# Performance work log

Measured on AMD Instinct MI355X. Metric: run time of the kernel, lower is better.

The kernel has to match this reference:

```python
import jax, jax.numpy as jnp
import numpy as np

B, T, E = 1024, 200, 128
H = 64

def setup_inputs() -> dict:
    key = jax.random.key(0)
    k1, k2, k3, k4 = jax.random.split(key, 4)
    return {
        "query": jax.random.normal(k1, (B, 1, E), dtype=jnp.float32),
        "keys": jax.random.normal(k2, (B, T, E), dtype=jnp.float32),
        "W0": jax.random.normal(k3, (4 * E, H), dtype=jnp.float32) * 0.05,
        "b0": jnp.zeros((H,), dtype=jnp.float32),
        "W1": jax.random.normal(k4, (H, 1), dtype=jnp.float32) * 0.05,
        "b1": jnp.zeros((1,), dtype=jnp.float32),
    }

def reference(query, keys, W0, b0, W1, b1):
    # query: [B,1,E] broadcast to [B,T,E] (repeat_elements along axis 1)
    q = jnp.broadcast_to(query, keys.shape)
    # dnn_input: [B,T,4E] = concat([q, k, q-k, q*k])
    x = jnp.concatenate([q, keys, q - keys, q * keys], axis=-1)
    # one hidden layer with relu, then linear scorer -> [B,T,1]
    h = jax.nn.relu(jnp.einsum('btd,dh->bth', x, W0) + b0)
    att_score = jnp.einsum('bth,ho->bto', h, W1) + b1
    return att_score
```

## Files before the change

### kernel.cpp

```cpp
#include <hip/hip_runtime.h>
#include <hip/hip_bf16.h>


#define TB 200
#define EB 128
#define HB 64

typedef __attribute__((ext_vector_type(8))) short bf16x8;
typedef __attribute__((ext_vector_type(4))) float f32x4;

__global__ __launch_bounds__(256, 4)
void lau_kernel(const float* __restrict__ query,
                const float* __restrict__ keys,
                const float* __restrict__ W0,
                const float* __restrict__ b0,
                const float* __restrict__ W1,
                const float* __restrict__ b1,
                float* __restrict__ out)
{
    const int b    = blockIdx.x;
    const int tid  = threadIdx.x;
    const int lane = tid & 63;
    const int wave = tid >> 6;
    const int ln15 = lane & 15;
    const int quad = lane >> 4;

    __shared__ float bias_s[HB];
    __shared__ float w1_s[HB];
    __shared__ float red2[HB][17];
    __shared__ __align__(16) __hip_bfloat16 wbt[HB][EB + 8];

    const float* kb = keys + (size_t)b * TB * EB;

    {
        const int hq = (tid & 15) * 4;
        const int ck = tid >> 4;
        const float4 q0 = *(const float4*)&query[(size_t)b * EB + ck * 8];
        const float4 q1 = *(const float4*)&query[(size_t)b * EB + ck * 8 + 4];
        const float qe_arr[8] = {q0.x, q0.y, q0.z, q0.w, q1.x, q1.y, q1.z, q1.w};
        float bp0 = 0.f, bp1 = 0.f, bp2 = 0.f, bp3 = 0.f;
        #pragma unroll
        for (int i = 0; i < 8; ++i) {
            const int e = ck * 8 + i;
            const float qe = qe_arr[i];
            const float4 wa = *(const float4*)&W0[(size_t)e            * HB + hq];
            const float4 wb = *(const float4*)&W0[(size_t)(EB + e)     * HB + hq];
            const float4 wc = *(const float4*)&W0[(size_t)(2 * EB + e) * HB + hq];
            const float4 wd = *(const float4*)&W0[(size_t)(3 * EB + e) * HB + hq];
            wbt[hq + 0][e] = __float2bfloat16(wb.x - wc.x + qe * wd.x);
            wbt[hq + 1][e] = __float2bfloat16(wb.y - wc.y + qe * wd.y);
            wbt[hq + 2][e] = __float2bfloat16(wb.z - wc.z + qe * wd.z);
            wbt[hq + 3][e] = __float2bfloat16(wb.w - wc.w + qe * wd.w);
            bp0 += qe * (wa.x + wc.x);
            bp1 += qe * (wa.y + wc.y);
            bp2 += qe * (wa.z + wc.z);
            bp3 += qe * (wa.w + wc.w);
        }
        red2[hq + 0][ck] = bp0;
        red2[hq + 1][ck] = bp1;
        red2[hq + 2][ck] = bp2;
        red2[hq + 3][ck] = bp3;
    }

    float4 af[8];
    {
        const int mrow = wave * 16 + ln15;
        const float* arow = kb + (size_t)mrow * EB + quad * 8;
        #pragma unroll
        for (int ks = 0; ks < 4; ++ks) {
            af[2*ks]   = *(const float4*)(arow + ks * 32);
            af[2*ks+1] = *(const float4*)(arow + ks * 32 + 4);
        }
    }
    __syncthreads();

    if (tid < HB) {
        float s = b0[tid];
        #pragma unroll
        for (int c = 0; c < 16; ++c) s += red2[tid][c];
        bias_s[tid] = s;
        w1_s[tid]   = W1[tid];
    }
    __syncthreads();

    float w1q[4], biasq[4];
    #pragma unroll
    for (int nt = 0; nt < 4; ++nt) {
        w1q[nt]   = w1_s[nt * 16 + ln15];
        biasq[nt] = bias_s[nt * 16 + ln15];
    }

    const __hip_bfloat16* wb_base = &wbt[ln15][quad * 8];
    const float b1v = b1[0];

    for (int mt = wave; mt < 13; mt += 4) {
        bf16x8 ab[4];
        #pragma unroll
        for (int ks = 0; ks < 4; ++ks) {
            union { bf16x8 v; __hip_bfloat162 h2[4]; } u;
            u.h2[0] = __float22bfloat162_rn(make_float2(af[2*ks].x,   af[2*ks].y));
            u.h2[1] = __float22bfloat162_rn(make_float2(af[2*ks].z,   af[2*ks].w));
            u.h2[2] = __float22bfloat162_rn(make_float2(af[2*ks+1].x, af[2*ks+1].y));
            u.h2[3] = __float22bfloat162_rn(make_float2(af[2*ks+1].z, af[2*ks+1].w));
            ab[ks] = u.v;
        }

        if (mt + 4 < 13) {
            const int mrow = (mt + 4) * 16 + ln15;
            const int mc   = mrow < TB ? mrow : TB - 1;
            const float* arow = kb + (size_t)mc * EB + quad * 8;
            #pragma unroll
            for (int ks = 0; ks < 4; ++ks) {
                af[2*ks]   = *(const float4*)(arow + ks * 32);
                af[2*ks+1] = *(const float4*)(arow + ks * 32 + 4);
            }
        }

        f32x4 acc[4] = {{0,0,0,0},{0,0,0,0},{0,0,0,0},{0,0,0,0}};
        #pragma unroll
        for (int ks = 0; ks < 4; ++ks) {
            #pragma unroll
            for (int nt = 0; nt < 4; ++nt) {
                const bf16x8 bf = *(const bf16x8*)(wb_base + nt * 16 * (EB + 8) + ks * 32);
                acc[nt] = __builtin_amdgcn_mfma_f32_16x16x32_bf16(ab[ks], bf, acc[nt], 0, 0, 0);
            }
        }

        float part[4];
        #pragma unroll
        for (int r = 0; r < 4; ++r) {
            float s = 0.f;
            #pragma unroll
            for (int nt = 0; nt < 4; ++nt) {
                float hv = acc[nt][r] + biasq[nt];
                hv = hv > 0.f ? hv : 0.f;
                s += hv * w1q[nt];
            }
            part[r] = s;
        }
        #pragma unroll
        for (int m = 1; m < 16; m <<= 1) {
            #pragma unroll
            for (int r = 0; r < 4; ++r)
                part[r] += __shfl_xor(part[r], m, 64);
        }
        if (ln15 == 0) {
            #pragma unroll
            for (int r = 0; r < 4; ++r) {
                const int mg = mt * 16 + quad * 4 + r;
                if (mg < TB) out[(size_t)b * TB + mg] = part[r] + b1v;
            }
        }
    }
}

extern "C" void kernel_launch(void* const* d_in, const int* in_sizes, int n_in,
                              void* d_out, int out_size, void* d_ws, size_t ws_size,
                              hipStream_t stream) {
    const float* query = (const float*)d_in[0];
    const float* keys  = (const float*)d_in[1];
    const float* W0    = (const float*)d_in[2];
    const float* b0    = (const float*)d_in[3];
    const float* W1    = (const float*)d_in[4];
    const float* b1    = (const float*)d_in[5];
    float* out = (float*)d_out;

    lau_kernel<<<1024, 256, 0, stream>>>(query, keys, W0, b0, W1, b1, out);
}
```

Measured before the change: 181.0 us.

## Split weight folding into separate kernel and halve per-batch score blocks

Moves the per-batch query-folded W0 computation into its own kernel that writes bf16 weights and bias to a workspace. The scoring kernel then runs two blocks per batch, each handling about half of the 13 row tiles, and reloads the folded weights from the workspace. The aim is more parallelism, with the fold work kept off the critical path of the key-streaming GEMM. In exchange it adds a second launch, roughly 18MB of extra workspace traffic, and drops the software prefetch of the next key tile.

```diff
diff --git a/kernel.cpp b/kernel.cpp
--- a/kernel.cpp
+++ b/kernel.cpp
@@ -5,32 +5,23 @@
 #define TB 200
 #define EB 128
 #define HB 64
+#define WS_STRIDE 17664
 
 typedef __attribute__((ext_vector_type(8))) short bf16x8;
 typedef __attribute__((ext_vector_type(4))) float f32x4;
 
 __global__ __launch_bounds__(256, 4)
-void lau_kernel(const float* __restrict__ query,
-                const float* __restrict__ keys,
-                const float* __restrict__ W0,
-                const float* __restrict__ b0,
-                const float* __restrict__ W1,
-                const float* __restrict__ b1,
-                float* __restrict__ out)
+void fold_kernel(const float* __restrict__ query,
+                 const float* __restrict__ W0,
+                 const float* __restrict__ b0,
+                 unsigned char* __restrict__ ws)
 {
-    const int b    = blockIdx.x;
-    const int tid  = threadIdx.x;
-    const int lane = tid & 63;
-    const int wave = tid >> 6;
-    const int ln15 = lane & 15;
-    const int quad = lane >> 4;
+    const int b   = blockIdx.x;
+    const int tid = threadIdx.x;
 
+    __shared__ float red2[HB][17];
     __shared__ float bias_s[HB];
-    __shared__ float w1_s[HB];
-    __shared__ float red2[HB][17];
     __shared__ __align__(16) __hip_bfloat16 wbt[HB][EB + 8];
-
-    const float* kb = keys + (size_t)b * TB * EB;
 
     {
         const int hq = (tid & 15) * 4;
@@ -61,24 +52,50 @@
         red2[hq + 2][ck] = bp2;
         red2[hq + 3][ck] = bp3;
     }
-
-    float4 af[8];
-    {
-        const int mrow = wave * 16 + ln15;
-        const float* arow = kb + (size_t)mrow * EB + quad * 8;
-        #pragma unroll
-        for (int ks = 0; ks < 4; ++ks) {
-            af[2*ks]   = *(const float4*)(arow + ks * 32);
-            af[2*ks+1] = *(const float4*)(arow + ks * 32 + 4);
-        }
-    }
     __syncthreads();
-
     if (tid < HB) {
         float s = b0[tid];
         #pragma unroll
         for (int c = 0; c < 16; ++c) s += red2[tid][c];
         bias_s[tid] = s;
+    }
+    __syncthreads();
+
+    uint4* dst = (uint4*)(ws + (size_t)b * WS_STRIDE);
+    const uint4* srcW = (const uint4*)&wbt[0][0];
+    #pragma unroll
+    for (int k = 0; k < 4; ++k) dst[tid + k * 256] = srcW[tid + k * 256];
+    if (tid < 64) dst[1024 + tid] = srcW[1024 + tid];
+    if (tid < 16) dst[1088 + tid] = ((const uint4*)bias_s)[tid];
+}
+
+__global__ __launch_bounds__(256, 8)
+void score_kernel(const float* __restrict__ keys,
+                  const float* __restrict__ W1,
+                  const float* __restrict__ b1,
+                  const unsigned char* __restrict__ ws,
+                  float* __restrict__ out)
+{
+    const int bid  = blockIdx.x;
+    const int b    = bid >> 1;
+    const int half = bid & 1;
+    const int tid  = threadIdx.x;
+    const int lane = tid & 63;
+    const int wave = tid >> 6;
+    const int ln15 = lane & 15;
+    const int quad = lane >> 4;
+
+    __shared__ float bias_s[HB];
+    __shared__ float w1_s[HB];
+    __shared__ __align__(16) __hip_bfloat16 wbt[HB][EB + 8];
+
+    const uint4* src = (const uint4*)(ws + (size_t)b * WS_STRIDE);
+    uint4* dstW = (uint4*)&wbt[0][0];
+    #pragma unroll
+    for (int k = 0; k < 4; ++k) dstW[tid + k * 256] = src[tid + k * 256];
+    if (tid < 64) dstW[1024 + tid] = src[1024 + tid];
+    if (tid < 64) {
+        bias_s[tid] = ((const float*)(ws + (size_t)b * WS_STRIDE + 17408))[tid];
         w1_s[tid]   = W1[tid];
     }
     __syncthreads();
@@ -91,9 +108,21 @@
     }
 
     const __hip_bfloat16* wb_base = &wbt[ln15][quad * 8];
-    const float b1v = b1[0];
+    const float* kb  = keys + (size_t)b * TB * EB;
+    const float  b1v = b1[0];
 
-    for (int mt = wave; mt < 13; mt += 4) {
+    const int mtEnd = half ? 13 : 7;
+    for (int mt = half * 7 + wave; mt < mtEnd; mt += 4) {
+        const int mrow = mt * 16 + ln15;
+        const int mc   = mrow < TB ? mrow : TB - 1;
+        const float* arow = kb + (size_t)mc * EB + quad * 8;
+
+        float4 af[8];
+        #pragma unroll
+        for (int ks = 0; ks < 4; ++ks) {
+            af[2*ks]   = *(const float4*)(arow + ks * 32);
+            af[2*ks+1] = *(const float4*)(arow + ks * 32 + 4);
+        }
         bf16x8 ab[4];
         #pragma unroll
         for (int ks = 0; ks < 4; ++ks) {
@@ -103,17 +132,6 @@
             u.h2[2] = __float22bfloat162_rn(make_float2(af[2*ks+1].x, af[2*ks+1].y));
             u.h2[3] = __float22bfloat162_rn(make_float2(af[2*ks+1].z, af[2*ks+1].w));
             ab[ks] = u.v;
-        }
-
-        if (mt + 4 < 13) {
-            const int mrow = (mt + 4) * 16 + ln15;
-            const int mc   = mrow < TB ? mrow : TB - 1;
-            const float* arow = kb + (size_t)mc * EB + quad * 8;
-            #pragma unroll
-            for (int ks = 0; ks < 4; ++ks) {
-                af[2*ks]   = *(const float4*)(arow + ks * 32);
-                af[2*ks+1] = *(const float4*)(arow + ks * 32 + 4);
-            }
         }
 
         f32x4 acc[4] = {{0,0,0,0},{0,0,0,0},{0,0,0,0},{0,0,0,0}};
@@ -164,6 +182,8 @@
     const float* W1    = (const float*)d_in[4];
     const float* b1    = (const float*)d_in[5];
     float* out = (float*)d_out;
+    unsigned char* ws = (unsigned char*)d_ws;
 
-    lau_kernel<<<1024, 256, 0, stream>>>(query, keys, W0, b0, W1, b1, out);
+    fold_kernel<<<1024, 256, 0, stream>>>(query, W0, b0, ws);
+    score_kernel<<<2048, 256, 0, stream>>>(keys, W1, b1, ws, out);
 }
```

Result: slower. 219.4 us (+21.2%).
